# Kernel optimization log

Measured on AMD Instinct MI355X. Metric: run time of the kernel, lower is better.

## Reference

```python
import jax, jax.numpy as jnp
import numpy as np

# dims: R ranks, B batch, HQ q-heads, HKV kv-heads-per-rank, G = HQ//HKV group size,
# D head dim, S kv splits (hardcoded 32 in module), L max kv len per rank, P pages per rank
R, B, HQ, HKV, D, S, L, P = 4, 16, 32, 2, 128, 32, 2048, 32768
G = HQ // HKV  # kv_group_num = num_q_heads // num_kv_heads_per_rank
NEG = -jnp.inf


def setup_inputs() -> dict:
    key = jax.random.key(0)
    k1, k2, k3, k4, k5 = jax.random.split(key, 5)
    q = jax.random.normal(k1, (B, HQ, D), jnp.float32)
    k_cache = jax.random.normal(k2, (R, P, HKV, D), jnp.float32)
    v_cache = jax.random.normal(k3, (R, P, HKV, D), jnp.float32)
    block_table = jax.random.randint(k4, (R, B, L), 0, P, jnp.int32)
    # per-rank kv lengths; min 64 to keep all math well-defined
    kv_lens_per_rank = jax.random.randint(k5, (R, B), 64, L + 1, jnp.int32)
    return dict(q=q, k_cache=k_cache, v_cache=v_cache,
                block_table=block_table, kv_lens_per_rank=kv_lens_per_rank)


def _attend(q, k_cache, v_cache, block_table, kv_lens):
    scale = D ** -0.5
    # page_size == 1: block_table entries are token slots in the per-rank cache.
    ridx = jnp.arange(R)[:, None, None]
    k = k_cache[ridx, block_table]  # [R,B,L,HKV,D]
    v = v_cache[ridx, block_table]  # [R,B,L,HKV,D]

    # GQA: q head h uses local kv head h // G on each rank
    qg = q.reshape(B, HKV, G, D)
    scores = jnp.einsum('bkgd,rblkd->rbkgl', qg, k) * scale  # [R,B,HKV,G,L]

    n = jnp.arange(L)
    valid = n[None, None, :] < kv_lens[..., None]            # [R,B,L]
    scores = jnp.where(valid[:, :, None, None, :], scores, NEG)

    # stage 1: split-KV. split s covers [s*per, (s+1)*per) with per = ceil(len/S)
    per = -(-kv_lens // S)                                   # [R,B]
    sid = n[None, None, :] // per[..., None]                 # [R,B,L]

    lse_s = []
    for s in range(S):  # fixed small loop over NUM_KV_SPLITS
        m = jnp.where((sid == s)[:, :, None, None, :], scores, NEG)
        lse_s.append(jax.scipy.special.logsumexp(m, axis=-1))  # [R,B,HKV,G]
    lse_s = jnp.stack(lse_s)  # [S,R,B,HKV,G]; empty splits -> -inf (kernel skips them)

    # stage 2: local combine over splits. NOTE (faithful to kernel): local_out stores
    # the UNNORMALIZED accumulator sum_s exp(lse_s - m_r) * o_s together with
    # lse_r = m_r + log(sum_s exp(lse_s - m_r)), where m_r = max_s lse_s.
    m_r = jnp.max(lse_s, axis=0)                              # [R,B,HKV,G]
    lse_r = m_r + jnp.log(jnp.sum(jnp.exp(lse_s - m_r), axis=0))
    # sum_s exp(lse_s - m_r) * (softmax_s @ v_s) == sum_n exp(score_n - m_r) * v_n
    p = jnp.exp(scores - m_r[..., None])                      # masked entries -> 0
    acc_r = jnp.einsum('rbkgl,rblkd->rbkgd', p, v)            # [R,B,HKV,G,D]

    acc = acc_r.reshape(R, B, HQ, D)
    lse = lse_r.reshape(R, B, HQ)

    # stage 3: global lse-weighted combine across ranks (online softmax == this)
    M = jnp.max(lse, axis=0)                                  # [B,HQ]
    w = jnp.exp(lse - M)                                      # [R,B,HQ]
    out = jnp.sum(w[..., None] * acc, axis=0) / jnp.sum(w, axis=0)[..., None]
    return out  # [B,HQ,D]


def reference(q, k_cache, v_cache, block_table, kv_lens_per_rank):
    return _attend(q, k_cache, v_cache, block_table, kv_lens_per_rank)
```

## Files before the change

kernel.cpp:

```cpp
#include <hip/hip_runtime.h>
#include <math.h>

#define R_ 4
#define B_ 16
#define HQ_ 32
#define HKV_ 2
#define G_ 16
#define D_ 128
#define S_ 32
#define CT_ 32
#define L_ 2048
#define P_ 32768
#define KSTR 136
#define PSTR 20
#define NEGINF (-INFINITY)

typedef _Float16 h4 __attribute__((ext_vector_type(4)));
typedef _Float16 h8 __attribute__((ext_vector_type(8)));
typedef float    fx4 __attribute__((ext_vector_type(4)));


__global__ __launch_bounds__(128, 6) void fd_stage1(
    const float* __restrict__ q, const float* __restrict__ kc,
    const float* __restrict__ vc, const int* __restrict__ bt,
    const int* __restrict__ lens,
    float* __restrict__ pm_ws, float* __restrict__ se_ws,
    _Float16* __restrict__ chunk_acc)
{
  const int t   = threadIdx.x;
  const int blk = blockIdx.x;
  const int c   = blk >> 12;
  const int s   = (blk >> 7) & 31;
  const int rb  = (blk >> 1) & 63;
  const int hkv = blk & 1;
  const int r   = rb >> 4, b = rb & 15;

  const int len = lens[rb];
  const int per = (len + 31) >> 5;
  const int sn0 = s*per;
  const int stn = min(per, len - sn0);
  const int n0  = sn0 + c*CT_;
  const int tn  = min(stn - c*CT_, CT_);

  const int widx = ((rb*HKV_ + hkv)*S_ + s)*2 + c;
  float* pm_out = pm_ws + widx*G_;
  float* se_out = se_ws + widx*G_;
  _Float16* ca  = chunk_acc + (size_t)widx*(G_*D_);

  if (tn <= 0) {
    if (t < G_) { pm_out[t] = NEGINF; se_out[t] = 0.f; }
    h8 z = {};
    *(h8*)&ca[t*16]     = z;
    *(h8*)&ca[t*16 + 8] = z;
    return;
  }

  __shared__ _Float16 q_s[G_][KSTR];
  __shared__ __align__(16) float p_s[CT_][PSTR];
  __shared__ int      pg_s[CT_];
  __shared__ float2   red_s[2][G_];

  const int* btb = bt + rb*L_;
  const float* kvk = kc + (size_t)r*(P_*HKV_*D_) + hkv*D_;
  const float* kvv = vc + (size_t)r*(P_*HKV_*D_) + hkv*D_;

  if (t < CT_) pg_s[t] = btb[n0 + t];

  {
    const float* qb = q + (b*HQ_ + hkv*G_)*D_;
    int fi = t;
    #pragma unroll
    for (int i = 0; i < 4; ++i, fi += 128) {
      const int g = fi >> 5, dd = (fi & 31)*4;
      const float4 v = *(const float4*)&qb[g*D_ + dd];
      h4 hv; hv.x=(_Float16)v.x; hv.y=(_Float16)v.y; hv.z=(_Float16)v.z; hv.w=(_Float16)v.w;
      *(h4*)&q_s[g][dd] = hv;
    }
  }
  __syncthreads();

  const int w  = t >> 6;
  const int l  = t & 63;
  const int hh = l & 15;
  const int tq = l >> 4;
  const bool active = (16*w) < tn;

  fx4 d0 = {0.f,0.f,0.f,0.f};
  if (active) {
    const int row = 16*w + hh;
    const bool rowok = row < tn;
    const int pg = pg_s[row];
    const float* kr = kvk + pg*(HKV_*D_) + 8*tq;
    #pragma unroll
    for (int cc = 0; cc < 4; ++cc) {
      h8 af = {};
      if (rowok) {
        const float4 f0 = *(const float4*)&kr[cc*32];
        const float4 f1 = *(const float4*)&kr[cc*32 + 4];
        af[0]=(_Float16)f0.x; af[1]=(_Float16)f0.y; af[2]=(_Float16)f0.z; af[3]=(_Float16)f0.w;
        af[4]=(_Float16)f1.x; af[5]=(_Float16)f1.y; af[6]=(_Float16)f1.z; af[7]=(_Float16)f1.w;
      }
      const h8 bf = *(const h8*)&q_s[hh][cc*32 + 8*tq];
      d0 = __builtin_amdgcn_mfma_f32_16x16x32_f16(af, bf, d0, 0, 0, 0);
    }
  }

  const float sc = 0.08838834764831845f;
  const int nb = 16*w + 4*tq;
  const float sv0 = (nb+0 < tn) ? d0[0]*sc : NEGINF;
  const float sv1 = (nb+1 < tn) ? d0[1]*sc : NEGINF;
  const float sv2 = (nb+2 < tn) ? d0[2]*sc : NEGINF;
  const float sv3 = (nb+3 < tn) ? d0[3]*sc : NEGINF;

  float pmw = fmaxf(fmaxf(sv0, sv1), fmaxf(sv2, sv3));
  pmw = fmaxf(pmw, __shfl_xor(pmw, 16));
  pmw = fmaxf(pmw, __shfl_xor(pmw, 32));
  const float pms = (pmw == NEGINF) ? 0.f : pmw;
  const float e0 = __expf(sv0 - pms);
  const float e1 = __expf(sv1 - pms);
  const float e2 = __expf(sv2 - pms);
  const float e3 = __expf(sv3 - pms);
  float psw = e0 + e1 + e2 + e3;
  psw += __shfl_xor(psw, 16);
  psw += __shfl_xor(psw, 32);

  if (l < 16) red_s[w][l] = make_float2(pmw, psw);
  __syncthreads();

  const float2 r0 = red_s[0][hh], r1 = red_s[1][hh];
  const float pm = fmaxf(r0.x, r1.x);
  const float ps = r0.y*__expf(r0.x - pm) + r1.y*__expf(r1.x - pm);

  if (w == 0 && l < 16) {
    pm_out[l] = pm;
    se_out[l] = ps;
  }

  if (active) {
    const float cw = __expf(pmw - pm);
    p_s[nb+0][hh] = e0*cw;
    p_s[nb+1][hh] = e1*cw;
    p_s[nb+2][hh] = e2*cw;
    p_s[nb+3][hh] = e3*cw;
  }
  __syncthreads();

  const int d4 = (t & 31)*4;
  const int g4 = (t >> 5)*4;
  const float* vb = kvv + d4;
  float4 a0 = make_float4(0,0,0,0), a1 = make_float4(0,0,0,0);
  float4 a2 = make_float4(0,0,0,0), a3 = make_float4(0,0,0,0);
  #pragma unroll 4
  for (int n = 0; n < tn; ++n) {
    const int pg = pg_s[n];
    const float4 v4 = *(const float4*)&vb[pg*(HKV_*D_)];
    const float4 pp = *(const float4*)&p_s[n][g4];
    a0.x += pp.x*v4.x; a0.y += pp.x*v4.y; a0.z += pp.x*v4.z; a0.w += pp.x*v4.w;
    a1.x += pp.y*v4.x; a1.y += pp.y*v4.y; a1.z += pp.y*v4.z; a1.w += pp.y*v4.w;
    a2.x += pp.z*v4.x; a2.y += pp.z*v4.y; a2.z += pp.z*v4.z; a2.w += pp.z*v4.w;
    a3.x += pp.w*v4.x; a3.y += pp.w*v4.y; a3.z += pp.w*v4.z; a3.w += pp.w*v4.w;
  }

  h4 o;
  o.x=(_Float16)a0.x; o.y=(_Float16)a0.y; o.z=(_Float16)a0.z; o.w=(_Float16)a0.w;
  *(h4*)&ca[(g4+0)*D_ + d4] = o;
  o.x=(_Float16)a1.x; o.y=(_Float16)a1.y; o.z=(_Float16)a1.z; o.w=(_Float16)a1.w;
  *(h4*)&ca[(g4+1)*D_ + d4] = o;
  o.x=(_Float16)a2.x; o.y=(_Float16)a2.y; o.z=(_Float16)a2.z; o.w=(_Float16)a2.w;
  *(h4*)&ca[(g4+2)*D_ + d4] = o;
  o.x=(_Float16)a3.x; o.y=(_Float16)a3.y; o.z=(_Float16)a3.z; o.w=(_Float16)a3.w;
  *(h4*)&ca[(g4+3)*D_ + d4] = o;
}

__global__ __launch_bounds__(128) void fd_stage2(
    const float* __restrict__ pm_ws, const float* __restrict__ se_ws,
    const _Float16* __restrict__ chunk_acc, float* __restrict__ out)
{
  const int bh  = blockIdx.x;
  const int b   = bh >> 5, h = bh & 31;
  const int hkv = h >> 4, g = h & 31 & 15;
  const int d   = threadIdx.x;

  float lse_r[R_], a_r[R_];
  #pragma unroll
  for (int r = 0; r < R_; ++r) {
    const int base = ((r*B_ + b)*HKV_ + hkv)*(S_*2);
    const float* pmb = pm_ws + base*G_ + g;
    const float* seb = se_ws + base*G_ + g;

    float m = NEGINF;
    #pragma unroll 8
    for (int s2 = 0; s2 < S_; ++s2) {
      const float pm0 = pmb[(2*s2    )*G_];
      const float pm1 = pmb[(2*s2 + 1)*G_];
      const float se0 = seb[(2*s2    )*G_];
      const float se1 = seb[(2*s2 + 1)*G_];
      const float pmx = fmaxf(pm0, pm1);
      const float pmsafe = (pmx == NEGINF) ? 0.f : pmx;
      const float tt = se0*__expf(pm0 - pmsafe) + se1*__expf(pm1 - pmsafe);
      m = fmaxf(m, pmx + __logf(tt));
    }

    float sum = 0.f, a = 0.f;
    const _Float16* cab = chunk_acc + (size_t)base*(G_*D_) + g*D_ + d;
    #pragma unroll 8
    for (int sc2 = 0; sc2 < S_*2; ++sc2) {
      const float wc = __expf(pmb[sc2*G_] - m);
      sum += seb[sc2*G_] * wc;
      a   += wc * (float)cab[(size_t)sc2*(G_*D_)];
    }
    lse_r[r] = m + __logf(sum);
    a_r[r]   = a;
  }

  const float M = fmaxf(fmaxf(lse_r[0], lse_r[1]), fmaxf(lse_r[2], lse_r[3]));
  float denom = 0.f, o = 0.f;
  #pragma unroll
  for (int r = 0; r < R_; ++r) {
    const float w = __expf(lse_r[r] - M);
    denom += w;
    o += w * a_r[r];
  }
  out[(size_t)bh*D_ + d] = o / denom;
}

extern "C" void kernel_launch(void* const* d_in, const int* in_sizes, int n_in,
                              void* d_out, int out_size, void* d_ws, size_t ws_size,
                              hipStream_t stream) {
  const float* q   = (const float*)d_in[0];
  const float* kc  = (const float*)d_in[1];
  const float* vc  = (const float*)d_in[2];
  const int*   bt  = (const int*)d_in[3];
  const int*   len = (const int*)d_in[4];
  float* out = (float*)d_out;
  float* ws  = (float*)d_ws;

  const size_t nt = (size_t)R_*B_*HKV_*S_*2;
  float*    pm_ws     = ws;
  float*    se_ws     = ws + nt*G_;
  _Float16* chunk_acc = (_Float16*)(ws + 2*nt*G_);

  fd_stage1<<<dim3(2*S_*64*HKV_ ), dim3(128), 0, stream>>>(
      q, kc, vc, bt, len, pm_ws, se_ws, chunk_acc);
  fd_stage2<<<dim3(B_*HQ_), dim3(128), 0, stream>>>(
      pm_ws, se_ws, chunk_acc, out);
}
```

Measured before the change: 305.7 us.

## Parallelize combine kernel across ranks and skip empty second chunks

The combine kernel now runs 512 threads per block, one group of 128 per rank, instead of looping over the four ranks serially in each thread. The per-rank results are merged through shared memory. The workspace is reordered so each rank's chunk-0 and chunk-1 partials are contiguous, which lets the kernel read only the first chunk when the per-split length fits in one chunk. This cuts serial latency and loads in the combine stage, at the cost of a shared-memory sync and a read of the lengths array.

```diff
diff --git a/kernel.cpp b/kernel.cpp
--- a/kernel.cpp
+++ b/kernel.cpp
@@ -42,7 +42,7 @@
   const int n0  = sn0 + c*CT_;
   const int tn  = min(stn - c*CT_, CT_);
 
-  const int widx = ((rb*HKV_ + hkv)*S_ + s)*2 + c;
+  const int widx = ((rb*HKV_ + hkv)*2 + c)*S_ + s;
   float* pm_out = pm_ws + widx*G_;
   float* se_out = se_ws + widx*G_;
   _Float16* ca  = chunk_acc + (size_t)widx*(G_*D_);
@@ -172,56 +172,70 @@
   *(h4*)&ca[(g4+3)*D_ + d4] = o;
 }
 
-__global__ __launch_bounds__(128) void fd_stage2(
+__global__ __launch_bounds__(512) void fd_stage2(
     const float* __restrict__ pm_ws, const float* __restrict__ se_ws,
-    const _Float16* __restrict__ chunk_acc, float* __restrict__ out)
+    const _Float16* __restrict__ chunk_acc, const int* __restrict__ lens,
+    float* __restrict__ out)
 {
   const int bh  = blockIdx.x;
   const int b   = bh >> 5, h = bh & 31;
-  const int hkv = h >> 4, g = h & 31 & 15;
-  const int d   = threadIdx.x;
-
-  float lse_r[R_], a_r[R_];
-  #pragma unroll
-  for (int r = 0; r < R_; ++r) {
-    const int base = ((r*B_ + b)*HKV_ + hkv)*(S_*2);
-    const float* pmb = pm_ws + base*G_ + g;
-    const float* seb = se_ws + base*G_ + g;
-
-    float m = NEGINF;
+  const int hkv = h >> 4, g = h & 15;
+  const int t   = threadIdx.x;
+  const int r   = t >> 7;
+  const int d   = t & 127;
+
+  __shared__ float lse_s[R_];
+  __shared__ float a_s[R_][D_];
+
+  const int rb  = r*B_ + b;
+  const int len = lens[rb];
+  const int per = (len + 31) >> 5;
+  const bool two = per > 32;
+
+  const int cbase = (rb*HKV_ + hkv)*2*S_;
+  const float* pm0b = pm_ws + cbase*G_ + g;
+  const float* se0b = se_ws + cbase*G_ + g;
+  const float* pm1b = pm0b + S_*G_;
+  const float* se1b = se0b + S_*G_;
+
+  float m = NEGINF;
+  if (two) {
     #pragma unroll 8
-    for (int s2 = 0; s2 < S_; ++s2) {
-      const float pm0 = pmb[(2*s2    )*G_];
-      const float pm1 = pmb[(2*s2 + 1)*G_];
-      const float se0 = seb[(2*s2    )*G_];
-      const float se1 = seb[(2*s2 + 1)*G_];
+    for (int s = 0; s < S_; ++s) {
+      const float pm0 = pm0b[s*G_], pm1 = pm1b[s*G_];
+      const float se0 = se0b[s*G_], se1 = se1b[s*G_];
       const float pmx = fmaxf(pm0, pm1);
-      const float pmsafe = (pmx == NEGINF) ? 0.f : pmx;
-      const float tt = se0*__expf(pm0 - pmsafe) + se1*__expf(pm1 - pmsafe);
+      const float tt = se0*__expf(pm0 - pmx) + se1*__expf(pm1 - pmx);
       m = fmaxf(m, pmx + __logf(tt));
     }
-
-    float sum = 0.f, a = 0.f;
-    const _Float16* cab = chunk_acc + (size_t)base*(G_*D_) + g*D_ + d;
+  } else {
     #pragma unroll 8
-    for (int sc2 = 0; sc2 < S_*2; ++sc2) {
-      const float wc = __expf(pmb[sc2*G_] - m);
-      sum += seb[sc2*G_] * wc;
-      a   += wc * (float)cab[(size_t)sc2*(G_*D_)];
-    }
-    lse_r[r] = m + __logf(sum);
-    a_r[r]   = a;
-  }
-
-  const float M = fmaxf(fmaxf(lse_r[0], lse_r[1]), fmaxf(lse_r[2], lse_r[3]));
-  float denom = 0.f, o = 0.f;
-  #pragma unroll
-  for (int r = 0; r < R_; ++r) {
-    const float w = __expf(lse_r[r] - M);
-    denom += w;
-    o += w * a_r[r];
-  }
-  out[(size_t)bh*D_ + d] = o / denom;
+    for (int s = 0; s < S_; ++s)
+      m = fmaxf(m, pm0b[s*G_] + __logf(se0b[s*G_]));
+  }
+
+  const int nsc = two ? 2*S_ : S_;
+  float sum = 0.f, a = 0.f;
+  const _Float16* cab = chunk_acc + (size_t)cbase*(G_*D_) + g*D_ + d;
+  #pragma unroll 8
+  for (int sc2 = 0; sc2 < nsc; ++sc2) {
+    const float wc = __expf(pm0b[sc2*G_] - m);
+    sum += se0b[sc2*G_] * wc;
+    a   += wc * (float)cab[(size_t)sc2*(G_*D_)];
+  }
+
+  if (d == 0) lse_s[r] = m + __logf(sum);
+  a_s[r][d] = a;
+  __syncthreads();
+
+  if (t < D_) {
+    const float l0 = lse_s[0], l1 = lse_s[1], l2 = lse_s[2], l3 = lse_s[3];
+    const float M  = fmaxf(fmaxf(l0, l1), fmaxf(l2, l3));
+    const float w0 = __expf(l0 - M), w1 = __expf(l1 - M);
+    const float w2 = __expf(l2 - M), w3 = __expf(l3 - M);
+    const float o  = w0*a_s[0][t] + w1*a_s[1][t] + w2*a_s[2][t] + w3*a_s[3][t];
+    out[(size_t)bh*D_ + t] = o / (w0 + w1 + w2 + w3);
+  }
 }
 
 extern "C" void kernel_launch(void* const* d_in, const int* in_sizes, int n_in,
@@ -240,8 +254,8 @@
   float*    se_ws     = ws + nt*G_;
   _Float16* chunk_acc = (_Float16*)(ws + 2*nt*G_);
 
-  fd_stage1<<<dim3(2*S_*64*HKV_ ), dim3(128), 0, stream>>>(
+  fd_stage1<<<dim3(8192), dim3(128), 0, stream>>>(
       q, kc, vc, bt, len, pm_ws, se_ws, chunk_acc);
-  fd_stage2<<<dim3(B_*HQ_), dim3(128), 0, stream>>>(
-      pm_ws, se_ws, chunk_acc, out);
+  fd_stage2<<<dim3(B_*HQ_), dim3(512), 0, stream>>>(
+      pm_ws, se_ws, chunk_acc, len, out);
 }
```

Result: faster. 282.6 us (-7.5%).
